# Performance work log

Measured on AMD Instinct MI355X. Metric: run time of the kernel, lower is better.

The kernel has to match this reference:

```python
import jax, jax.numpy as jnp
import numpy as np

B, T, C = 4, 2048, 1024
H = 16
HD = C // H  # 64


def setup_inputs() -> dict:
    key = jax.random.key(0)
    ks = jax.random.split(key, 4)
    x = jax.random.normal(ks[0], (B, T, C), dtype=jnp.float32)
    # c_attn: Linear(C, 3C, bias=False)  (qkv_bias=False)
    w_attn = jax.random.normal(ks[1], (C, 3 * C), dtype=jnp.float32) / np.sqrt(C)
    # c_proj: Linear(C, C) with bias (nn.Linear default)
    w_proj = jax.random.normal(ks[2], (C, C), dtype=jnp.float32) / np.sqrt(C)
    b_proj = jax.random.normal(ks[3], (C,), dtype=jnp.float32) * 0.01
    return {"x": x, "w_attn": w_attn, "w_proj": w_proj, "b_proj": b_proj}


def reference(x, w_attn, w_proj, b_proj):
    b, t, c = x.shape
    qkv = x @ w_attn  # [B,T,3C]
    q, k, v = jnp.split(qkv, 3, axis=-1)
    # [B,H,T,HD]
    q = q.reshape(b, t, H, HD).transpose(0, 2, 1, 3)
    k = k.reshape(b, t, H, HD).transpose(0, 2, 1, 3)
    v = v.reshape(b, t, H, HD).transpose(0, 2, 1, 3)
    scale = 1.0 / np.sqrt(HD)
    attn = jnp.einsum('bhqd,bhkd->bhqk', q, k) * scale  # [B,H,T,T]
    causal = jnp.tril(jnp.ones((t, t), dtype=bool))
    attn = jnp.where(causal, attn, -jnp.inf)
    attn = jax.nn.softmax(attn, axis=-1)
    out = jnp.einsum('bhqk,bhkd->bhqd', attn, v)  # [B,H,T,HD]
    out = out.transpose(0, 2, 1, 3).reshape(b, t, c)
    return out @ w_proj + b_proj
```

## Files before the change

kernel.cpp:

```cpp
#include <hip/hip_runtime.h>

#define BB 4
#define TT 2048
#define CC 1024
#define C3 3072
#define HH 16
#define HD 64
#define BT 8192

#define TS 32
#define TSZ (64 * TS)

typedef __bf16 bf16x8 __attribute__((ext_vector_type(8)));
typedef float floatx4 __attribute__((ext_vector_type(4)));
typedef unsigned uintx2 __attribute__((ext_vector_type(2)));
typedef unsigned short u16;

__device__ __forceinline__ u16 f2bf(float f) {
  union { float f; unsigned u; } a; a.f = f;
  return (u16)((a.u + 0x7fffu + ((a.u >> 16) & 1u)) >> 16);
}
__device__ __forceinline__ bf16x8 ld8(const u16* p) { return *(const bf16x8*)p; }
__device__ __forceinline__ floatx4 mfma16(bf16x8 a, bf16x8 b, floatx4 c) {
  return __builtin_amdgcn_mfma_f32_16x16x32_bf16(a, b, c, 0, 0, 0);
}

__device__ __forceinline__ void gload16(const u16* g, u16* l) {
  __builtin_amdgcn_global_load_lds(
      (const __attribute__((address_space(1))) void*)g,
      (__attribute__((address_space(3))) void*)l, 16, 0, 0);
}

__device__ __forceinline__ void qd_xchg(unsigned a, unsigned b,
                                        unsigned& r0, unsigned& r1) {
  uintx2 t = __builtin_amdgcn_permlane32_swap(a, b, false, false);
  uintx2 r = __builtin_amdgcn_permlane16_swap(t[0], t[1], false, false);
  r0 = r[0]; r1 = r[1];
}

#define BARR do { asm volatile("" ::: "memory"); \
                  __builtin_amdgcn_s_barrier(); \
                  asm volatile("" ::: "memory"); } while (0)
#define VMW4 asm volatile("s_waitcnt vmcnt(4)" ::: "memory")
#define VMW0 asm volatile("s_waitcnt vmcnt(0)" ::: "memory")

__global__ __launch_bounds__(256) void prep_kernel(
    const float4* __restrict__ x4, ushort4* __restrict__ xb4,
    const float* __restrict__ w_attn, u16* __restrict__ waT,
    const float* __restrict__ w_proj, u16* __restrict__ wpT) {
  __shared__ float s[64][65];
  const int t = threadIdx.x;
  const int bid = blockIdx.x;

  if (bid < 8192) {
    const int i = bid * 256 + t;
    float4 v = x4[i];
    ushort4 o; o.x = f2bf(v.x); o.y = f2bf(v.y); o.z = f2bf(v.z); o.w = f2bf(v.w);
    xb4[i] = o;
    return;
  }

  const float* src; u16* dst; int N, bx, by;
  if (bid < 8960) { const int b2 = bid - 8192; src = w_attn; dst = waT; N = C3;
                    bx = b2 % 48; by = b2 / 48; }
  else            { const int b2 = bid - 8960; src = w_proj; dst = wpT; N = CC;
                    bx = b2 % 16; by = b2 / 16; }
  const int K = CC;
  const int r = t >> 4;
  const int c = (t & 15) * 4;
  const int k0 = by * 64, n0 = bx * 64;
#pragma unroll
  for (int i = 0; i < 4; ++i) {
    float4 v = *(const float4*)&src[(size_t)(k0 + r + i * 16) * N + n0 + c];
    s[r + i * 16][c + 0] = v.x; s[r + i * 16][c + 1] = v.y;
    s[r + i * 16][c + 2] = v.z; s[r + i * 16][c + 3] = v.w;
  }
  __syncthreads();
#pragma unroll
  for (int i = 0; i < 4; ++i) {
    const int nn = r + i * 16;
    ushort4 o;
    o.x = f2bf(s[c + 0][nn]); o.y = f2bf(s[c + 1][nn]);
    o.z = f2bf(s[c + 2][nn]); o.w = f2bf(s[c + 3][nn]);
    *(ushort4*)&dst[(size_t)(n0 + nn) * K + k0 + c] = o;
  }
}

template<int MODE>
__global__ __launch_bounds__(512, 2) void gemm256_kernel(
    const u16* __restrict__ A, const u16* __restrict__ B,
    const float* __restrict__ bias, float* __restrict__ outf,
    u16* __restrict__ qk, u16* __restrict__ vT, int N, int K) {
  __shared__ u16 lds[2][24576];

  const int t = threadIdx.x;
  const int lane = t & 63, lr = lane & 15, qd = lane >> 4;
  const int w = t >> 6, wm = w >> 1, wn = w & 1;
  const int m0 = blockIdx.y * 256, n0 = blockIdx.x * 128;

  const int srow = t >> 3;
  const int scol = ((t & 7) ^ (srow & 7)) * 8;
  const u16* Asrc = A + (size_t)(m0 + srow) * K + scol;
  const u16* Bsrc = B + (size_t)(n0 + srow) * K + scol;
  const int wvb = (t & ~63) * 8;

  const int NT = K >> 6;
  floatx4 acc[4][4] = {};

  const int abase = (wm * 64 + lr) * 64;
  const int bbase = (wn * 64 + lr) * 64;
  const int csw0 = (qd * 8) ^ ((lr & 7) * 8);
  const int csw1 = (32 + qd * 8) ^ ((lr & 7) * 8);

#define STG_A(PR, QA, TK) do { if ((TK) < NT) \
    gload16(Asrc + (size_t)((QA) * 64) * K + (TK) * 64, \
            &lds[PR][(QA) * 4096 + wvb]); } while (0)
#define STG_B(PR, HB, TK) do { if ((TK) < NT) \
    gload16(Bsrc + (size_t)((HB) * 64) * K + (TK) * 64, \
            &lds[PR][16384 + (HB) * 4096 + wvb]); } while (0)

  bf16x8 af[4][2], bf[2][2];
#define READ_A(PR) do { _Pragma("unroll") for (int mi = 0; mi < 4; ++mi) { \
    const u16* p_ = &lds[PR][mi * 1024 + abase]; \
    af[mi][0] = ld8(p_ + csw0); af[mi][1] = ld8(p_ + csw1); } } while (0)
#define READ_B(PR, NJ0) do { _Pragma("unroll") for (int nj = 0; nj < 2; ++nj) { \
    const u16* p_ = &lds[PR][16384 + ((NJ0) + nj) * 1024 + bbase]; \
    bf[nj][0] = ld8(p_ + csw0); bf[nj][1] = ld8(p_ + csw1); } } while (0)
#define MFMA16(NJ0) do { __builtin_amdgcn_s_setprio(1); _Pragma("unroll") \
    for (int mi = 0; mi < 4; ++mi) _Pragma("unroll") for (int nj = 0; nj < 2; ++nj) { \
      acc[mi][(NJ0) + nj] = mfma16(af[mi][0], bf[nj][0], acc[mi][(NJ0) + nj]); \
      acc[mi][(NJ0) + nj] = mfma16(af[mi][1], bf[nj][1], acc[mi][(NJ0) + nj]); } \
    __builtin_amdgcn_s_setprio(0); } while (0)

  STG_A(0, 0, 0); STG_A(0, 1, 0); STG_A(0, 2, 0); STG_A(0, 3, 0);
  STG_B(0, 0, 0); STG_B(0, 1, 0);
  STG_A(1, 0, 1); STG_A(1, 1, 1); STG_A(1, 2, 1); STG_A(1, 3, 1);
  VMW4; BARR;

  const int NITER = NT >> 1;
  for (int it = 0; it < NITER; ++it) {
    const int T1 = 2 * it + 1, T2 = 2 * it + 2, T3 = 2 * it + 3;
    const bool last = (it == NITER - 1);
    STG_B(1, 0, T1); STG_B(1, 1, T1);
    READ_A(0); READ_B(0, 0); MFMA16(0);
    BARR;
    STG_A(0, 0, T2); STG_A(0, 1, T2); STG_A(0, 2, T2); STG_A(0, 3, T2);
    READ_B(0, 2); MFMA16(2);
    if (last) { VMW0; } else { VMW4; }
    BARR;
    STG_B(0, 0, T2); STG_B(0, 1, T2);
    READ_A(1); READ_B(1, 0); MFMA16(0);
    BARR;
    STG_A(1, 0, T3); STG_A(1, 1, T3); STG_A(1, 2, T3); STG_A(1, 3, T3);
    READ_B(1, 2); MFMA16(2);
    if (last) { VMW0; } else { VMW4; }
    BARR;
  }
#undef STG_A
#undef STG_B
#undef READ_A
#undef READ_B
#undef MFMA16

  u16* flat = &lds[0][0];
  if constexpr (MODE == 2) {
    const int rowg0 = m0 + wm * 64;
    const int colg0 = n0 + wn * 64;
#pragma unroll
    for (int nj = 0; nj < 4; ++nj) {
      const int col = colg0 + nj * 16 + lr;
      const float bv = bias[col];
#pragma unroll
      for (int mi = 0; mi < 4; ++mi)
#pragma unroll
        for (int i = 0; i < 4; ++i)
          outf[(size_t)(rowg0 + mi * 16 + qd * 4 + i) * N + col] = acc[mi][nj][i] + bv;
    }
  } else {
    const bool isV = (n0 >= 2 * CC);
    if (!isV) {
      const float qs = (n0 < CC) ? 0.18033688011f : 1.0f;
      u16* Tw = flat + w * (32 * 72);
      const int C0 = n0 + wn * 64;
#pragma unroll
      for (int mi2 = 0; mi2 < 2; ++mi2) {
#pragma unroll
        for (int mh = 0; mh < 2; ++mh)
#pragma unroll
          for (int nj = 0; nj < 4; ++nj)
#pragma unroll
            for (int i = 0; i < 4; ++i)
              Tw[(mh * 16 + qd * 4 + i) * 72 + nj * 16 + lr] =
                  f2bf(acc[mi2 * 2 + mh][nj][i] * qs);
        const int R0 = m0 + wm * 64 + mi2 * 32;
#pragma unroll
        for (int s = 0; s < 4; ++s) {
          const int rl = s * 8 + (lane >> 3);
          const int c0 = (lane & 7) * 8;
          *(bf16x8*)&qk[(size_t)(R0 + rl) * (2 * CC) + C0 + c0] =
              ld8(&Tw[rl * 72 + c0]);
        }
      }
    } else {
      u16* Tv = flat + w * (64 * 72);
      const int bI = m0 >> 11;
      const int tbase = (m0 & (TT - 1)) + wm * 64;
      const int dim0 = (n0 - 2 * CC) + wn * 64;
#pragma unroll
      for (int nj = 0; nj < 4; ++nj)
#pragma unroll
        for (int mi = 0; mi < 4; ++mi)
#pragma unroll
          for (int i = 0; i < 4; ++i)
            Tv[(nj * 16 + lr) * 72 + mi * 16 + qd * 4 + i] =
                f2bf(acc[mi][nj][i]);
#pragma unroll
      for (int s = 0; s < 8; ++s) {
        const int dl = s * 8 + (lane >> 3);
        const int t0 = (lane & 7) * 8;
        *(bf16x8*)&vT[((size_t)(bI << 10) + dim0 + dl) * TT + tbase + t0] =
            ld8(&Tv[dl * 72 + t0]);
      }
    }
  }
}

template<int MODE>
__global__ __launch_bounds__(256) void gemm_kernel(
    const u16* __restrict__ A, const u16* __restrict__ B,
    const float* __restrict__ bias, float* __restrict__ outf,
    int M, int N, int K) {
  __shared__ u16 smem[2][2][2 * TSZ];

  const int t = threadIdx.x;
  const int w = t >> 6, lane = t & 63, lr = lane & 15, qd = lane >> 4;
  const int wm = w >> 1, wn = w & 1;
  const int m0 = blockIdx.y * 128, n0 = blockIdx.x * 128;

  const int sr = t >> 2;
  const int sc = (t & 3) * 8;
  const int wb = (t & ~63) * 8;
  const u16* Ag = A + (size_t)(m0 + sr) * K + sc;
  const u16* Bg = B + (size_t)(n0 + sr) * K + sc;

  floatx4 acc[4][4] = {};

  {
    u16* sA = &smem[0][0][0];
    u16* sB = &smem[0][1][0];
    gload16(Ag,                  &sA[wb]);
    gload16(Ag + (size_t)64 * K, &sA[TSZ + wb]);
    gload16(Bg,                  &sB[wb]);
    gload16(Bg + (size_t)64 * K, &sB[TSZ + wb]);
  }
  __syncthreads();

  for (int k0 = 0; k0 < K; k0 += 32) {
    const int p = (k0 >> 5) & 1;
    if (k0 + 32 < K) {
      u16* sA = &smem[p ^ 1][0][0];
      u16* sB = &smem[p ^ 1][1][0];
      gload16(Ag + k0 + 32,                  &sA[wb]);
      gload16(Ag + (size_t)64 * K + k0 + 32, &sA[TSZ + wb]);
      gload16(Bg + k0 + 32,                  &sB[wb]);
      gload16(Bg + (size_t)64 * K + k0 + 32, &sB[TSZ + wb]);
    }
    const u16* sA = &smem[p][0][0];
    const u16* sB = &smem[p][1][0];

    bf16x8 af[4], bf[4];
#pragma unroll
    for (int mj = 0; mj < 4; ++mj) af[mj] = ld8(&sA[(wm * 64 + mj * 16 + lr) * TS + qd * 8]);
#pragma unroll
    for (int nj = 0; nj < 4; ++nj) bf[nj] = ld8(&sB[(wn * 64 + nj * 16 + lr) * TS + qd * 8]);
#pragma unroll
    for (int mj = 0; mj < 4; ++mj)
#pragma unroll
      for (int nj = 0; nj < 4; ++nj)
        acc[mj][nj] = mfma16(af[mj], bf[nj], acc[mj][nj]);
    __syncthreads();
  }

  const int rowg0 = m0 + wm * 64;
  const int colg0 = n0 + wn * 64;
#pragma unroll
  for (int nj = 0; nj < 4; ++nj) {
    const int col = colg0 + nj * 16 + lr;
    const float bv = bias[col];
#pragma unroll
    for (int mj = 0; mj < 4; ++mj)
#pragma unroll
      for (int i = 0; i < 4; ++i)
        outf[(size_t)(rowg0 + mj * 16 + qd * 4 + i) * N + col] = acc[mj][nj][i] + bv;
  }
}

__global__ __launch_bounds__(256, 5) void attn_kernel(const u16* __restrict__ qk,
                                                      const u16* __restrict__ vT,
                                                      u16* __restrict__ att) {
  __shared__ u16 sKV[2][4][TSZ];

  const int t = threadIdx.x;
  const int w = t >> 6, lane = t & 63, lr = lane & 15, qd = lane >> 4;
  const int qtile = 31 - blockIdx.y;
  const int bh = blockIdx.x;
  const int b = bh >> 4, h = bh & 15;
  const int q0 = qtile * 64;
  const u16* qbase = qk + (size_t)b * TT * (2 * CC);

  const u16* qp = qbase + (size_t)(q0 + w * 16 + lr) * (2 * CC) + h * HD;
  const bf16x8 qf0 = ld8(qp + qd * 8);
  const bf16x8 qf1 = ld8(qp + 32 + qd * 8);

  const int sr = t >> 2, sc = (t & 3) * 8;
  const int wb = (t & ~63) * 8;
  const u16* Kg = qbase + (size_t)sr * (2 * CC) + CC + h * HD + sc;
  const u16* Vg = vT + ((size_t)bh * HD + sr) * TT + sc;

  float lsum = 0.f;
  floatx4 o[4] = {};
  const int myq = q0 + w * 16 + lr;

  {
    u16* b0 = &sKV[0][0][0];
    gload16(Kg,      &b0[wb]);
    gload16(Kg + 32, &b0[TSZ + wb]);
    gload16(Vg,      &b0[2 * TSZ + wb]);
    gload16(Vg + 32, &b0[3 * TSZ + wb]);
  }
  __syncthreads();

  for (int kt = 0; kt <= qtile; ++kt) {
    if (kt < qtile) {
      const int kn = (kt + 1) * 64;
      u16* bn = &sKV[(kt + 1) & 1][0][0];
      gload16(Kg + (size_t)kn * (2 * CC),      &bn[wb]);
      gload16(Kg + (size_t)kn * (2 * CC) + 32, &bn[TSZ + wb]);
      gload16(Vg + kn,                         &bn[2 * TSZ + wb]);
      gload16(Vg + kn + 32,                    &bn[3 * TSZ + wb]);
    }

    const u16* sK0 = &sKV[kt & 1][0][0];
    const u16* sK1 = &sKV[kt & 1][1][0];
    const u16* sV0 = &sKV[kt & 1][2][0];
    const u16* sV1 = &sKV[kt & 1][3][0];

    floatx4 s[4] = {};
#pragma unroll
    for (int j = 0; j < 4; ++j) {
      bf16x8 kf0 = ld8(&sK0[(j * 16 + lr) * TS + qd * 8]);
      bf16x8 kf1 = ld8(&sK1[(j * 16 + lr) * TS + qd * 8]);
      s[j] = mfma16(kf0, qf0, s[j]);
      s[j] = mfma16(kf1, qf1, s[j]);
    }

    const bool diag = (kt == qtile);
    unsigned W[4][2];
#pragma unroll
    for (int j = 0; j < 4; ++j) {
      float p[4];
#pragma unroll
      for (int i = 0; i < 4; ++i) {
        p[i] = __builtin_amdgcn_exp2f(s[j][i]);
        if (diag) {
          const int key = kt * 64 + j * 16 + qd * 4 + i;
          p[i] = (key <= myq) ? p[i] : 0.f;
        }
        lsum += p[i];
      }
      W[j][0] = __builtin_amdgcn_perm(__float_as_uint(p[1]), __float_as_uint(p[0]), 0x07060302);
      W[j][1] = __builtin_amdgcn_perm(__float_as_uint(p[3]), __float_as_uint(p[2]), 0x07060302);
    }

    uint4 F0, F1;
    qd_xchg(W[0][0], W[1][0], F0.x, F0.z);
    qd_xchg(W[0][1], W[1][1], F0.y, F0.w);
    qd_xchg(W[2][0], W[3][0], F1.x, F1.z);
    qd_xchg(W[2][1], W[3][1], F1.y, F1.w);
    const bf16x8 pf0 = __builtin_bit_cast(bf16x8, F0);
    const bf16x8 pf1 = __builtin_bit_cast(bf16x8, F1);

#pragma unroll
    for (int j = 0; j < 4; ++j) {
      bf16x8 vf0 = ld8(&sV0[(j * 16 + lr) * TS + qd * 8]);
      bf16x8 vf1 = ld8(&sV1[(j * 16 + lr) * TS + qd * 8]);
      o[j] = mfma16(pf0, vf0, o[j]);
      o[j] = mfma16(pf1, vf1, o[j]);
    }
    __syncthreads();
  }

  lsum += __shfl_xor(lsum, 16);
  lsum += __shfl_xor(lsum, 32);
  float linv[4];
#pragma unroll
  for (int i = 0; i < 4; ++i) linv[i] = 1.0f / __shfl(lsum, qd * 4 + i);

#pragma unroll
  for (int j = 0; j < 4; ++j)
#pragma unroll
    for (int i = 0; i < 4; ++i) {
      const size_t row = (size_t)b * TT + q0 + w * 16 + qd * 4 + i;
      att[row * CC + h * HD + j * 16 + lr] = f2bf(o[j][i] * linv[i]);
    }
}

extern "C" void kernel_launch(void* const* d_in, const int* in_sizes, int n_in,
                              void* d_out, int out_size, void* d_ws, size_t ws_size,
                              hipStream_t stream) {
  const float* x      = (const float*)d_in[0];
  const float* w_attn = (const float*)d_in[1];
  const float* w_proj = (const float*)d_in[2];
  const float* b_proj = (const float*)d_in[3];
  float* out = (float*)d_out;

  char* ws = (char*)d_ws;
  u16* xb  = (u16*)(ws + 0);
  u16* waT = (u16*)(ws + 16777216);
  u16* wpT = (u16*)(ws + 23068672);
  u16* qk  = (u16*)(ws + 25165824);
  u16* vT  = (u16*)(ws + 58720256);
  u16* att = (u16*)(ws + 75497472);

  prep_kernel<<<9216, 256, 0, stream>>>((const float4*)x, (ushort4*)xb,
                                        w_attn, waT, w_proj, wpT);

  gemm256_kernel<1><<<dim3(24, 32), 512, 0, stream>>>(xb, waT, nullptr, nullptr,
                                                      qk, vT, C3, CC);

  attn_kernel<<<dim3(64, 32), 256, 0, stream>>>(qk, vT, att);

  gemm_kernel<2><<<dim3(8, 64), 256, 0, stream>>>(att, wpT, b_proj, out,
                                                  BT, CC, CC);
}
```

Measured before the change: 219.9 us.

## Enlarge QKV GEMM tile to 256x256 with 8-wave quadrant schedule and swizzled grid

Rewrites the QKV projection GEMM to use 256x256 output tiles per block: 8 waves in a 2x4 arrangement, each wave owning 128x64 of accumulators. K-tiles are staged in quarter-tile pieces interleaved with quadrant MFMA groups and explicit lgkm/vm waits. The 1D grid is remapped so consecutive blocks are spread across XCDs. The aim is more arithmetic per LDS/global load and better L2 locality, at the cost of doubled accumulator registers, extra barriers, and fewer blocks (384) to fill the GPU.

Result: slower. 231.6 us (+5.3%).

```diff
diff --git a/kernel.cpp b/kernel.cpp
--- a/kernel.cpp
+++ b/kernel.cpp
@@ -41,8 +41,10 @@
 #define BARR do { asm volatile("" ::: "memory"); \
                   __builtin_amdgcn_s_barrier(); \
                   asm volatile("" ::: "memory"); } while (0)
-#define VMW4 asm volatile("s_waitcnt vmcnt(4)" ::: "memory")
-#define VMW0 asm volatile("s_waitcnt vmcnt(0)" ::: "memory")
+#define VMW4  asm volatile("s_waitcnt vmcnt(4)" ::: "memory")
+#define VMW0  asm volatile("s_waitcnt vmcnt(0)" ::: "memory")
+#define VMNOP do {} while (0)
+#define LGKM0 asm volatile("s_waitcnt lgkmcnt(0)" ::: "memory")
 
 __global__ __launch_bounds__(256) void prep_kernel(
     const float4* __restrict__ x4, ushort4* __restrict__ xb4,
@@ -86,17 +88,16 @@
   }
 }
 
-template<int MODE>
-__global__ __launch_bounds__(512, 2) void gemm256_kernel(
+__global__ __launch_bounds__(512, 2) void qkv_kernel(
     const u16* __restrict__ A, const u16* __restrict__ B,
-    const float* __restrict__ bias, float* __restrict__ outf,
-    u16* __restrict__ qk, u16* __restrict__ vT, int N, int K) {
-  __shared__ u16 lds[2][24576];
+    u16* __restrict__ qk, u16* __restrict__ vT, int K) {
+  __shared__ u16 lds[2][4][8192];
 
   const int t = threadIdx.x;
   const int lane = t & 63, lr = lane & 15, qd = lane >> 4;
-  const int w = t >> 6, wm = w >> 1, wn = w & 1;
-  const int m0 = blockIdx.y * 256, n0 = blockIdx.x * 128;
+  const int w = t >> 6, wm = w >> 2, wn = w & 3;
+  const int L = (blockIdx.x & 7) * 48 + (blockIdx.x >> 3);
+  const int m0 = (L / 12) * 256, n0 = (L % 12) * 256;
 
   const int srow = t >> 3;
   const int scol = ((t & 7) ^ (srow & 7)) * 8;
@@ -105,127 +106,115 @@
   const int wvb = (t & ~63) * 8;
 
   const int NT = K >> 6;
-  floatx4 acc[4][4] = {};
-
-  const int abase = (wm * 64 + lr) * 64;
-  const int bbase = (wn * 64 + lr) * 64;
+  floatx4 acc[8][4] = {};
+
+  const int bh2 = wn >> 1, brow0 = (wn & 1) * 64;
   const int csw0 = (qd * 8) ^ ((lr & 7) * 8);
   const int csw1 = (32 + qd * 8) ^ ((lr & 7) * 8);
 
-#define STG_A(PR, QA, TK) do { if ((TK) < NT) \
-    gload16(Asrc + (size_t)((QA) * 64) * K + (TK) * 64, \
-            &lds[PR][(QA) * 4096 + wvb]); } while (0)
-#define STG_B(PR, HB, TK) do { if ((TK) < NT) \
-    gload16(Bsrc + (size_t)((HB) * 64) * K + (TK) * 64, \
-            &lds[PR][16384 + (HB) * 4096 + wvb]); } while (0)
-
-  bf16x8 af[4][2], bf[2][2];
-#define READ_A(PR) do { _Pragma("unroll") for (int mi = 0; mi < 4; ++mi) { \
-    const u16* p_ = &lds[PR][mi * 1024 + abase]; \
+#define STG(PR, HT, TK) do { \
+    const u16* g_ = (((HT) < 2) ? Asrc : Bsrc) + \
+                    (size_t)(((HT) & 1) * 128) * K + (size_t)(TK) * 64; \
+    u16* l_ = &lds[PR][HT][wvb]; \
+    gload16(g_, l_); \
+    gload16(g_ + (size_t)64 * K, l_ + 4096); } while (0)
+
+  bf16x8 af[4][2], bf0[2][2], bf1[2][2];
+#define READ_A(PR, QR) do { _Pragma("unroll") for (int mi = 0; mi < 4; ++mi) { \
+    const u16* p_ = &lds[PR][wm][((QR) * 64 + mi * 16 + lr) * 64]; \
     af[mi][0] = ld8(p_ + csw0); af[mi][1] = ld8(p_ + csw1); } } while (0)
-#define READ_B(PR, NJ0) do { _Pragma("unroll") for (int nj = 0; nj < 2; ++nj) { \
-    const u16* p_ = &lds[PR][16384 + ((NJ0) + nj) * 1024 + bbase]; \
-    bf[nj][0] = ld8(p_ + csw0); bf[nj][1] = ld8(p_ + csw1); } } while (0)
-#define MFMA16(NJ0) do { __builtin_amdgcn_s_setprio(1); _Pragma("unroll") \
-    for (int mi = 0; mi < 4; ++mi) _Pragma("unroll") for (int nj = 0; nj < 2; ++nj) { \
-      acc[mi][(NJ0) + nj] = mfma16(af[mi][0], bf[nj][0], acc[mi][(NJ0) + nj]); \
-      acc[mi][(NJ0) + nj] = mfma16(af[mi][1], bf[nj][1], acc[mi][(NJ0) + nj]); } \
+#define READ_B(PR, QC, BF) do { _Pragma("unroll") for (int nj = 0; nj < 2; ++nj) { \
+    const u16* p_ = &lds[PR][2 + bh2][(brow0 + (QC) * 32 + nj * 16 + lr) * 64]; \
+    BF[nj][0] = ld8(p_ + csw0); BF[nj][1] = ld8(p_ + csw1); } } while (0)
+#define MFMAQ(QR, QC, BF) do { __builtin_amdgcn_s_setprio(1); \
+    _Pragma("unroll") for (int mi = 0; mi < 4; ++mi) \
+    _Pragma("unroll") for (int nj = 0; nj < 2; ++nj) { \
+      acc[(QR)*4+mi][(QC)*2+nj] = mfma16(af[mi][0], BF[nj][0], acc[(QR)*4+mi][(QC)*2+nj]); \
+      acc[(QR)*4+mi][(QC)*2+nj] = mfma16(af[mi][1], BF[nj][1], acc[(QR)*4+mi][(QC)*2+nj]); } \
     __builtin_amdgcn_s_setprio(0); } while (0)
 
-  STG_A(0, 0, 0); STG_A(0, 1, 0); STG_A(0, 2, 0); STG_A(0, 3, 0);
-  STG_B(0, 0, 0); STG_B(0, 1, 0);
-  STG_A(1, 0, 1); STG_A(1, 1, 1); STG_A(1, 2, 1); STG_A(1, 3, 1);
+#define KTILE(T, P, Q, WEND) do { \
+    READ_A(P, 0); READ_B(P, 0, bf0); \
+    if ((T) + 1 < NT) STG(Q, 0, (T) + 1); \
+    BARR; LGKM0; MFMAQ(0, 0, bf0); BARR; \
+    READ_B(P, 1, bf1); \
+    if ((T) + 1 < NT) STG(Q, 1, (T) + 1); \
+    BARR; LGKM0; MFMAQ(0, 1, bf1); BARR; \
+    READ_A(P, 1); \
+    if ((T) + 2 < NT) STG(P, 2, (T) + 2); \
+    BARR; LGKM0; MFMAQ(1, 0, bf0); BARR; \
+    if ((T) + 2 < NT) STG(P, 3, (T) + 2); \
+    BARR; MFMAQ(1, 1, bf1); WEND; BARR; \
+  } while (0)
+
+  STG(0, 2, 0); STG(0, 3, 0);
+  STG(0, 0, 0); STG(0, 1, 0);
+  STG(1, 2, 1); STG(1, 3, 1);
   VMW4; BARR;
 
-  const int NITER = NT >> 1;
-  for (int it = 0; it < NITER; ++it) {
-    const int T1 = 2 * it + 1, T2 = 2 * it + 2, T3 = 2 * it + 3;
-    const bool last = (it == NITER - 1);
-    STG_B(1, 0, T1); STG_B(1, 1, T1);
-    READ_A(0); READ_B(0, 0); MFMA16(0);
-    BARR;
-    STG_A(0, 0, T2); STG_A(0, 1, T2); STG_A(0, 2, T2); STG_A(0, 3, T2);
-    READ_B(0, 2); MFMA16(2);
-    if (last) { VMW0; } else { VMW4; }
-    BARR;
-    STG_B(0, 0, T2); STG_B(0, 1, T2);
-    READ_A(1); READ_B(1, 0); MFMA16(0);
-    BARR;
-    STG_A(1, 0, T3); STG_A(1, 1, T3); STG_A(1, 2, T3); STG_A(1, 3, T3);
-    READ_B(1, 2); MFMA16(2);
-    if (last) { VMW0; } else { VMW4; }
-    BARR;
-  }
-#undef STG_A
-#undef STG_B
+  for (int T = 0; T < NT - 2; ++T) {
+    const int p = T & 1;
+    KTILE(T, p, p ^ 1, VMW4);
+  }
+  { const int p = (NT - 2) & 1; KTILE(NT - 2, p, p ^ 1, VMW0); }
+  { const int p = (NT - 1) & 1; KTILE(NT - 1, p, p ^ 1, VMNOP); }
+#undef STG
 #undef READ_A
 #undef READ_B
-#undef MFMA16
-
-  u16* flat = &lds[0][0];
-  if constexpr (MODE == 2) {
-    const int rowg0 = m0 + wm * 64;
-    const int colg0 = n0 + wn * 64;
-#pragma unroll
-    for (int nj = 0; nj < 4; ++nj) {
-      const int col = colg0 + nj * 16 + lr;
-      const float bv = bias[col];
-#pragma unroll
-      for (int mi = 0; mi < 4; ++mi)
-#pragma unroll
-        for (int i = 0; i < 4; ++i)
-          outf[(size_t)(rowg0 + mi * 16 + qd * 4 + i) * N + col] = acc[mi][nj][i] + bv;
+#undef MFMAQ
+#undef KTILE
+
+  u16* flat = &lds[0][0][0];
+  const bool isV = (n0 >= 2 * CC);
+  if (!isV) {
+    const float qs = (n0 < CC) ? 0.18033688011f : 1.0f;
+    u16* Tw = flat + w * (32 * 72);
+    const int C0 = n0 + wn * 64;
+#pragma unroll
+    for (int rg = 0; rg < 4; ++rg) {
+#pragma unroll
+      for (int fh = 0; fh < 2; ++fh)
+#pragma unroll
+        for (int nj = 0; nj < 4; ++nj)
+#pragma unroll
+          for (int i = 0; i < 4; ++i)
+            Tw[(fh * 16 + qd * 4 + i) * 72 + nj * 16 + lr] =
+                f2bf(acc[rg * 2 + fh][nj][i] * qs);
+      const int R0 = m0 + wm * 128 + rg * 32;
+#pragma unroll
+      for (int s = 0; s < 4; ++s) {
+        const int rl = s * 8 + (lane >> 3);
+        const int c0 = (lane & 7) * 8;
+        *(bf16x8*)&qk[(size_t)(R0 + rl) * (2 * CC) + C0 + c0] =
+            ld8(&Tw[rl * 72 + c0]);
+      }
     }
   } else {
-    const bool isV = (n0 >= 2 * CC);
-    if (!isV) {
-      const float qs = (n0 < CC) ? 0.18033688011f : 1.0f;
-      u16* Tw = flat + w * (32 * 72);
-      const int C0 = n0 + wn * 64;
-#pragma unroll
-      for (int mi2 = 0; mi2 < 2; ++mi2) {
-#pragma unroll
-        for (int mh = 0; mh < 2; ++mh)
-#pragma unroll
-          for (int nj = 0; nj < 4; ++nj)
-#pragma unroll
-            for (int i = 0; i < 4; ++i)
-              Tw[(mh * 16 + qd * 4 + i) * 72 + nj * 16 + lr] =
-                  f2bf(acc[mi2 * 2 + mh][nj][i] * qs);
-        const int R0 = m0 + wm * 64 + mi2 * 32;
-#pragma unroll
-        for (int s = 0; s < 4; ++s) {
-          const int rl = s * 8 + (lane >> 3);
-          const int c0 = (lane & 7) * 8;
-          *(bf16x8*)&qk[(size_t)(R0 + rl) * (2 * CC) + C0 + c0] =
-              ld8(&Tw[rl * 72 + c0]);
-        }
-      }
-    } else {
-      u16* Tv = flat + w * (64 * 72);
-      const int bI = m0 >> 11;
-      const int tbase = (m0 & (TT - 1)) + wm * 64;
-      const int dim0 = (n0 - 2 * CC) + wn * 64;
+    u16* Tv = flat + w * (64 * 72);
+    const int bI = m0 >> 11;
+    const int tbase = (m0 & (TT - 1)) + wm * 128;
+    const int dim0 = (n0 - 2 * CC) + wn * 64;
+#pragma unroll
+    for (int th = 0; th < 2; ++th) {
 #pragma unroll
       for (int nj = 0; nj < 4; ++nj)
 #pragma unroll
-        for (int mi = 0; mi < 4; ++mi)
+        for (int fh = 0; fh < 4; ++fh)
 #pragma unroll
           for (int i = 0; i < 4; ++i)
-            Tv[(nj * 16 + lr) * 72 + mi * 16 + qd * 4 + i] =
-                f2bf(acc[mi][nj][i]);
+            Tv[(nj * 16 + lr) * 72 + fh * 16 + qd * 4 + i] =
+                f2bf(acc[th * 4 + fh][nj][i]);
 #pragma unroll
       for (int s = 0; s < 8; ++s) {
         const int dl = s * 8 + (lane >> 3);
         const int t0 = (lane & 7) * 8;
-        *(bf16x8*)&vT[((size_t)(bI << 10) + dim0 + dl) * TT + tbase + t0] =
+        *(bf16x8*)&vT[((size_t)(bI << 10) + dim0 + dl) * TT + tbase + th * 64 + t0] =
             ld8(&Tv[dl * 72 + t0]);
       }
     }
   }
 }
 
-template<int MODE>
 __global__ __launch_bounds__(256) void gemm_kernel(
     const u16* __restrict__ A, const u16* __restrict__ B,
     const float* __restrict__ bias, float* __restrict__ outf,
@@ -425,11 +414,10 @@
   prep_kernel<<<9216, 256, 0, stream>>>((const float4*)x, (ushort4*)xb,
                                         w_attn, waT, w_proj, wpT);
 
-  gemm256_kernel<1><<<dim3(24, 32), 512, 0, stream>>>(xb, waT, nullptr, nullptr,
-                                                      qk, vT, C3, CC);
+  qkv_kernel<<<384, 512, 0, stream>>>(xb, waT, qk, vT, CC);
 
   attn_kernel<<<dim3(64, 32), 256, 0, stream>>>(qk, vT, att);
 
-  gemm_kernel<2><<<dim3(8, 64), 256, 0, stream>>>(att, wpT, b_proj, out,
-                                                  BT, CC, CC);
-}
+  gemm_kernel<<<dim3(8, 64), 256, 0, stream>>>(att, wpT, b_proj, out,
+                                               BT, CC, CC);
+}
```
